# Optimization experiments

Hardware: AMD Instinct MI355X
Metric: run time of the kernel (lower is better)

The kernel has to match this reference:

```python
import jax, jax.numpy as jnp
import numpy as np

G, DIN, DOUT, R = 8, 1024, 1024, 16
N = 8192
SCALE = 32.0 / 16.0  # alpha / r


def grouped_linear(x, W, mask):
    """Grouped linear: out[n] = x[n] @ W[g[n]].
    x: [N, din], W: [G, din, dout], mask: [N, G] one-hot (float).
    Computed as all-group matmul + select; the fused grouped-GEMM is the
    kernel opportunity this reference baselines."""
    y_all = jnp.einsum('ni,gio->gno', x, W)      # [G, N, dout]
    return jnp.einsum('gno,ng->no', y_all, mask)  # [N, dout]


def setup_inputs() -> dict:
    key = jax.random.key(0)
    k1, k2, k3, k4, k5 = jax.random.split(key, 5)
    x = jax.random.normal(k1, (N, DIN), dtype=jnp.float32)
    x_groups = jnp.sort(jax.random.randint(k2, (N,), 0, G, dtype=jnp.int64))
    W_base = jax.random.normal(k3, (G, DIN, DOUT), dtype=jnp.float32) * 0.02
    W_A = jax.random.normal(k4, (G, DIN, R), dtype=jnp.float32) * 0.02
    # original inits lora_B to zero; use small random values so the LoRA path
    # contributes nonzero signal for correctness testing
    W_B = jax.random.normal(k5, (G, R, DOUT), dtype=jnp.float32) * 0.02
    return {"x": x, "x_groups": x_groups, "W_base": W_base, "W_A": W_A, "W_B": W_B}


def reference(x, x_groups, W_base, W_A, W_B):
    mask = (x_groups[:, None] == jnp.arange(G)).astype(x.dtype)  # [N, G] one-hot
    base = grouped_linear(x, W_base, mask)            # base GroupedLinear
    a = grouped_linear(x, W_A, mask)                  # lora_A (dropout p=0 -> identity)
    adapt = grouped_linear(a, W_B, mask)              # lora_B
    return base + SCALE * adapt
```

## Files before the change

### kernel.cpp

```cpp
#include <hip/hip_runtime.h>
#include <stdint.h>

#define N_TOK 8192
#define DIN   1024
#define DOUT  1024
#define NG    8
#define LSCALE 2.0f

typedef __attribute__((ext_vector_type(4))) float  float4v;
typedef __attribute__((ext_vector_type(8))) short  short8;
typedef short8  frag_ab;
typedef float4v frag_cd;

__device__ __forceinline__ short f2bf(float f) {
    union { float f; uint32_t u; } v; v.f = f;
    uint32_t r = v.u + 0x7fffu + ((v.u >> 16) & 1u);
    return (short)(r >> 16);
}

__device__ __forceinline__ void load_lds16(const void* g, void* lds) {
    __builtin_amdgcn_global_load_lds(
        (const __attribute__((address_space(1))) uint32_t*)g,
        (__attribute__((address_space(3))) uint32_t*)lds,
        16, 0, 0);
}

#define PREP_GRID 6177

__global__ __launch_bounds__(256) void prep_kernel(
        const float* __restrict__ x, const float* __restrict__ Wb,
        const float* __restrict__ WA, const float* __restrict__ WB,
        const int* __restrict__ groups,
        short* __restrict__ xb, short* __restrict__ Wt,
        int* __restrict__ starts) {
    __shared__ float tile[64][65];
    __shared__ float At[64][17];
    __shared__ float Bt[16][64];
    const int blk = blockIdx.x, t = threadIdx.x;

    if (blk < 4096) {
        size_t idx = (size_t)(blk * 256 + t) * 8;
        const float4v* p = (const float4v*)(x + idx);
        float4v a = p[0], b = p[1];
        short8 o;
        o[0]=f2bf(a[0]); o[1]=f2bf(a[1]); o[2]=f2bf(a[2]); o[3]=f2bf(a[3]);
        o[4]=f2bf(b[0]); o[5]=f2bf(b[1]); o[6]=f2bf(b[2]); o[7]=f2bf(b[3]);
        *(short8*)(xb + idx) = o;
    } else if (blk < 6144) {
        int b = blk - 4096;
        int g = b >> 8, rem = b & 255;
        int n0 = (rem & 15) * 64, k0 = (rem >> 4) * 64;
        const float* Wg = Wb + (size_t)g * DIN * DOUT;
#pragma unroll
        for (int i = 0; i < 4; ++i) {
            int idx = i * 256 + t;
            int r = idx >> 4, c = (idx & 15) * 4;
            float4v v = *(const float4v*)(Wg + (size_t)(k0 + r) * DOUT + n0 + c);
            tile[r][c+0]=v[0]; tile[r][c+1]=v[1]; tile[r][c+2]=v[2]; tile[r][c+3]=v[3];
        }
        {
            int kk = t >> 2, c = (t & 3) * 4;
            float4v v = *(const float4v*)(WA + ((size_t)g * DIN + k0 + kk) * 16 + c);
            At[kk][c+0]=v[0]; At[kk][c+1]=v[1]; At[kk][c+2]=v[2]; At[kk][c+3]=v[3];
        }
        {
            int r = t >> 4, c = (t & 15) * 4;
            float4v v = *(const float4v*)(WB + ((size_t)g * 16 + r) * DOUT + n0 + c);
            Bt[r][c+0]=v[0]; Bt[r][c+1]=v[1]; Bt[r][c+2]=v[2]; Bt[r][c+3]=v[3];
        }
        __syncthreads();
        short* Wtg = Wt + (size_t)g * DOUT * DIN;
#pragma unroll
        for (int i = 0; i < 2; ++i) {
            int idx = i * 256 + t;
            int n = idx >> 3, c8 = (idx & 7) * 8;
            float corr[8] = {0.f,0.f,0.f,0.f,0.f,0.f,0.f,0.f};
#pragma unroll
            for (int r = 0; r < 16; ++r) {
                float bv = Bt[r][n];
#pragma unroll
                for (int j = 0; j < 8; ++j) corr[j] += At[c8 + j][r] * bv;
            }
            short8 o;
#pragma unroll
            for (int j = 0; j < 8; ++j)
                o[j] = f2bf(tile[c8 + j][n] + LSCALE * corr[j]);
            *(short8*)(Wtg + (size_t)(n0 + n) * DIN + k0 + c8) = o;
        }
    } else {
        int i = (blk - 6144) * 256 + t;
        if (i > N_TOK) return;
        int cur  = (i < N_TOK) ? groups[i] : NG;
        int prev = (i == 0) ? -1 : groups[i - 1];
        for (int g = prev + 1; g <= cur; ++g) starts[g] = i;
    }
}

#define BM 128
#define BN 128
#define BK 64
#define NKT (DIN / BK)
#define MAXRT (N_TOK / BM + NG - 1)
#define GRID  (MAXRT * (DOUT / BN))

__global__ __launch_bounds__(256, 2)
void gemm_grouped(const short* __restrict__ xb,
                  const short* __restrict__ Wt,
                  const int*   __restrict__ starts,
                  float* __restrict__ out) {
    __shared__ short As[2][BM * BK];
    __shared__ short Bs[2][BN * BK];

    const int t    = threadIdx.x;
    const int lane = t & 63;
    const int wid  = t >> 6;
    const int L  = blockIdx.x;
    const int wg = (L & 7) * MAXRT + (L >> 3);
    const int rt = wg >> 3;
    const int ct = wg & 7;
    const int col0 = ct * BN;

    int g = -1, row0 = 0, rhi = 0;
    {
        int accum = 0;
#pragma unroll
        for (int gg = 0; gg < NG; ++gg) {
            int s0 = starts[gg], s1 = starts[gg + 1];
            int nt = (s1 - s0 + BM - 1) >> 7;
            if (g < 0 && rt < accum + nt) {
                g = gg;
                row0 = s0 + (rt - accum) * BM;
                rhi = (s1 < row0 + BM) ? s1 : row0 + BM;
            }
            accum += nt;
        }
    }
    if (g < 0) return;

    const short* wgp = Wt + (size_t)g * DOUT * DIN;
    const int wr  = (wid >> 1) * 64;
    const int wc  = (wid & 1) * 64;
    const int m16 = lane & 15;
    const int q   = lane >> 4;
    const int phase = ((L >> 3) & 1) * 8;

    frag_cd acc[4][4];
#pragma unroll
    for (int i = 0; i < 4; ++i)
#pragma unroll
        for (int j = 0; j < 4; ++j) { frag_cd z = {0.f,0.f,0.f,0.f}; acc[i][j] = z; }

    auto STAGE = [&](int buf, int kt) {
#pragma unroll
        for (int i = 0; i < 4; ++i) {
            int Lc = i * 256 + t;
            int r  = Lc >> 3;
            int c8 = (Lc & 7) ^ (r & 7);
            load_lds16(xb + (size_t)(row0 + r) * DIN + kt + c8 * 8,
                       &As[buf][(i * 256 + wid * 64) * 8]);
        }
#pragma unroll
        for (int i = 0; i < 4; ++i) {
            int Lc = i * 256 + t;
            int r  = Lc >> 3;
            int c8 = (Lc & 7) ^ (r & 7);
            load_lds16(wgp + (size_t)(col0 + r) * DIN + kt + c8 * 8,
                       &Bs[buf][(i * 256 + wid * 64) * 8]);
        }
    };

    STAGE(0, ((0 + phase) & (NKT - 1)) * BK);
    __syncthreads();

    int cur = 0;
#pragma unroll 2
    for (int kt_ii = 0; kt_ii < NKT; ++kt_ii) {
        if (kt_ii + 1 < NKT)
            STAGE(cur ^ 1, ((kt_ii + 1 + phase) & (NKT - 1)) * BK);

#pragma unroll
        for (int kk = 0; kk < BK; kk += 32) {
            frag_ab af[4], bf[4];
            const int ch = (kk >> 3) + q;
#pragma unroll
            for (int mi = 0; mi < 4; ++mi) {
                int rr = wr + mi * 16 + m16;
                af[mi] = *(const frag_ab*)&As[cur][rr * BK + ((ch ^ (rr & 7)) << 3)];
            }
#pragma unroll
            for (int ni = 0; ni < 4; ++ni) {
                int cc = wc + ni * 16 + m16;
                bf[ni] = *(const frag_ab*)&Bs[cur][cc * BK + ((ch ^ (cc & 7)) << 3)];
            }
#pragma unroll
            for (int mi = 0; mi < 4; ++mi)
#pragma unroll
                for (int ni = 0; ni < 4; ++ni)
                    acc[mi][ni] = __builtin_amdgcn_mfma_f32_16x16x32_bf16(
                        af[mi], bf[ni], acc[mi][ni], 0, 0, 0);
        }

        __syncthreads();
        cur ^= 1;
    }

#pragma unroll
    for (int mi = 0; mi < 4; ++mi)
#pragma unroll
        for (int r = 0; r < 4; ++r) {
            int grow = row0 + wr + mi * 16 + q * 4 + r;
            if (grow < rhi) {
                float* orow = out + (size_t)grow * DOUT + col0 + wc + m16;
#pragma unroll
                for (int ni = 0; ni < 4; ++ni) orow[ni * 16] = acc[mi][ni][r];
            }
        }
}

extern "C" void kernel_launch(void* const* d_in, const int* in_sizes, int n_in,
                              void* d_out, int out_size, void* d_ws, size_t ws_size,
                              hipStream_t stream) {
    const float* x      = (const float*)d_in[0];
    const int*   groups = (const int*)d_in[1];
    const float* Wb     = (const float*)d_in[2];
    const float* WA     = (const float*)d_in[3];
    const float* WB     = (const float*)d_in[4];
    float* out = (float*)d_out;

    char* ws = (char*)d_ws;
    int*   starts = (int*)ws;
    short* xb     = (short*)(ws + 1024);
    short* Wt     = (short*)(ws + 1024 + (size_t)16 * 1024 * 1024);

    hipLaunchKernelGGL(prep_kernel, dim3(PREP_GRID), dim3(256), 0, stream,
                       x, Wb, WA, WB, groups, xb, Wt, starts);
    hipLaunchKernelGGL(gemm_grouped, dim3(GRID), dim3(256), 0, stream,
                       xb, Wt, starts, out);
}
```

Measured before the change: 155.5 us.

## Fuse fp32-to-bf16 conversion of x into grouped GEMM A-tile staging

Removes the separate pass that converts x to bf16 in workspace; the GEMM now loads fp32 x rows into registers, converts them, and writes swizzled bf16 into LDS after the MFMA block. This eliminates a full read/write pass over x and shrinks the prep kernel. In exchange, each GEMM block reads twice as many bytes for the A operand across the repeated column tiles, and holds extra registers that may affect occupancy.

```diff
diff --git a/kernel.cpp b/kernel.cpp
--- a/kernel.cpp
+++ b/kernel.cpp
@@ -25,30 +25,19 @@
         16, 0, 0);
 }
 
-#define PREP_GRID 6177
-
-__global__ __launch_bounds__(256) void prep_kernel(
-        const float* __restrict__ x, const float* __restrict__ Wb,
-        const float* __restrict__ WA, const float* __restrict__ WB,
-        const int* __restrict__ groups,
-        short* __restrict__ xb, short* __restrict__ Wt,
-        int* __restrict__ starts) {
+#define PREPW_GRID 2081
+
+__global__ __launch_bounds__(256) void prep_w(
+        const float* __restrict__ Wb, const float* __restrict__ WA,
+        const float* __restrict__ WB, const int* __restrict__ groups,
+        short* __restrict__ Wt, int* __restrict__ starts) {
     __shared__ float tile[64][65];
     __shared__ float At[64][17];
     __shared__ float Bt[16][64];
     const int blk = blockIdx.x, t = threadIdx.x;
 
-    if (blk < 4096) {
-        size_t idx = (size_t)(blk * 256 + t) * 8;
-        const float4v* p = (const float4v*)(x + idx);
-        float4v a = p[0], b = p[1];
-        short8 o;
-        o[0]=f2bf(a[0]); o[1]=f2bf(a[1]); o[2]=f2bf(a[2]); o[3]=f2bf(a[3]);
-        o[4]=f2bf(b[0]); o[5]=f2bf(b[1]); o[6]=f2bf(b[2]); o[7]=f2bf(b[3]);
-        *(short8*)(xb + idx) = o;
-    } else if (blk < 6144) {
-        int b = blk - 4096;
-        int g = b >> 8, rem = b & 255;
+    if (blk < 2048) {
+        int g = blk >> 8, rem = blk & 255;
         int n0 = (rem & 15) * 64, k0 = (rem >> 4) * 64;
         const float* Wg = Wb + (size_t)g * DIN * DOUT;
 #pragma unroll
@@ -88,7 +77,7 @@
             *(short8*)(Wtg + (size_t)(n0 + n) * DIN + k0 + c8) = o;
         }
     } else {
-        int i = (blk - 6144) * 256 + t;
+        int i = (blk - 2048) * 256 + t;
         if (i > N_TOK) return;
         int cur  = (i < N_TOK) ? groups[i] : NG;
         int prev = (i == 0) ? -1 : groups[i - 1];
@@ -104,7 +93,7 @@
 #define GRID  (MAXRT * (DOUT / BN))
 
 __global__ __launch_bounds__(256, 2)
-void gemm_grouped(const short* __restrict__ xb,
+void gemm_grouped(const float* __restrict__ x,
                   const short* __restrict__ Wt,
                   const int*   __restrict__ starts,
                   float* __restrict__ out) {
@@ -150,15 +139,33 @@
 #pragma unroll
         for (int j = 0; j < 4; ++j) { frag_cd z = {0.f,0.f,0.f,0.f}; acc[i][j] = z; }
 
-    auto STAGE = [&](int buf, int kt) {
+    float4v ar[8];
+    auto LOAD_A = [&](int kt) {
 #pragma unroll
         for (int i = 0; i < 4; ++i) {
             int Lc = i * 256 + t;
             int r  = Lc >> 3;
-            int c8 = (Lc & 7) ^ (r & 7);
-            load_lds16(xb + (size_t)(row0 + r) * DIN + kt + c8 * 8,
-                       &As[buf][(i * 256 + wid * 64) * 8]);
-        }
+            int c8 = Lc & 7;
+            int rg = row0 + r; rg = rg < N_TOK ? rg : N_TOK - 1;
+            const float4v* p = (const float4v*)(x + (size_t)rg * DIN + kt + c8 * 8);
+            ar[2*i]   = p[0];
+            ar[2*i+1] = p[1];
+        }
+    };
+    auto CVT_A = [&](int buf) {
+#pragma unroll
+        for (int i = 0; i < 4; ++i) {
+            int Lc = i * 256 + t;
+            int r  = Lc >> 3;
+            int c8 = Lc & 7;
+            float4v a = ar[2*i], b = ar[2*i+1];
+            short8 o;
+            o[0]=f2bf(a[0]); o[1]=f2bf(a[1]); o[2]=f2bf(a[2]); o[3]=f2bf(a[3]);
+            o[4]=f2bf(b[0]); o[5]=f2bf(b[1]); o[6]=f2bf(b[2]); o[7]=f2bf(b[3]);
+            *(short8*)&As[buf][r * BK + ((c8 ^ (r & 7)) << 3)] = o;
+        }
+    };
+    auto STAGE_B = [&](int buf, int kt) {
 #pragma unroll
         for (int i = 0; i < 4; ++i) {
             int Lc = i * 256 + t;
@@ -169,14 +176,23 @@
         }
     };
 
-    STAGE(0, ((0 + phase) & (NKT - 1)) * BK);
+    {
+        int kt0 = (phase & (NKT - 1)) * BK;
+        LOAD_A(kt0);
+        STAGE_B(0, kt0);
+        CVT_A(0);
+    }
     __syncthreads();
 
     int cur = 0;
 #pragma unroll 2
     for (int kt_ii = 0; kt_ii < NKT; ++kt_ii) {
-        if (kt_ii + 1 < NKT)
-            STAGE(cur ^ 1, ((kt_ii + 1 + phase) & (NKT - 1)) * BK);
+        const bool hasnext = (kt_ii + 1 < NKT);
+        if (hasnext) {
+            int ktn = ((kt_ii + 1 + phase) & (NKT - 1)) * BK;
+            LOAD_A(ktn);
+            STAGE_B(cur ^ 1, ktn);
+        }
 
 #pragma unroll
         for (int kk = 0; kk < BK; kk += 32) {
@@ -199,6 +215,8 @@
                     acc[mi][ni] = __builtin_amdgcn_mfma_f32_16x16x32_bf16(
                         af[mi], bf[ni], acc[mi][ni], 0, 0, 0);
         }
+
+        if (hasnext) CVT_A(cur ^ 1);
 
         __syncthreads();
         cur ^= 1;
@@ -229,11 +247,10 @@
 
     char* ws = (char*)d_ws;
     int*   starts = (int*)ws;
-    short* xb     = (short*)(ws + 1024);
-    short* Wt     = (short*)(ws + 1024 + (size_t)16 * 1024 * 1024);
-
-    hipLaunchKernelGGL(prep_kernel, dim3(PREP_GRID), dim3(256), 0, stream,
-                       x, Wb, WA, WB, groups, xb, Wt, starts);
+    short* Wt     = (short*)(ws + 1024);
+
+    hipLaunchKernelGGL(prep_w, dim3(PREPW_GRID), dim3(256), 0, stream,
+                       Wb, WA, WB, groups, Wt, starts);
     hipLaunchKernelGGL(gemm_grouped, dim3(GRID), dim3(256), 0, stream,
-                       xb, Wt, starts, out);
-}
+                       x, Wt, starts, out);
+}
```

Measured after the change: 158.0 us. No clear change (+1.6%).
